# Performance work log

Hardware: AMD Instinct MI355X
Metric: run time of the kernel (lower is better)

The kernel has to match this reference:

```python
import jax, jax.numpy as jnp
import numpy as np

B_T = 32      # input capsule types
C_T = 32      # output capsule types
K = 3         # conv kernel
STRIDE = 2
H = 4         # pose matrix side
HH = H * H
ITERS = 3
EPS = 1e-10
LN_2PI = np.float32(np.log(2.0 * np.pi))


def setup_inputs() -> dict:
    key = jax.random.key(0)
    k1, k2, k3, k4, k5 = jax.random.split(key, 5)
    b, win = 16, 14
    poses = jax.random.normal(k1, (b, HH * B_T, win, win), dtype=jnp.float32)
    activations = jax.random.uniform(k2, (b, B_T, win, win), dtype=jnp.float32)
    W = jax.random.normal(k3, (B_T, K, K, C_T, H, H), dtype=jnp.float32)
    beta_v = jax.random.normal(k4, (1, C_T, 1, 1), dtype=jnp.float32)
    beta_a = jax.random.normal(k5, (1, C_T, 1), dtype=jnp.float32)
    lambda_ = jnp.float32(0.01)
    return {"lambda_": lambda_, "poses": poses, "activations": activations,
            "W": W, "beta_v": beta_v, "beta_a": beta_a}


def _em_routing(lambda_, a_in, V, beta_v, beta_a, b, Bkk, Cww, ww):
    sg = jax.lax.stop_gradient
    R = jnp.full((b, Bkk, Cww), 1.0 / C_T, dtype=V.dtype)
    a = mu = None
    for i in range(ITERS):
        R4 = (R * a_in)[..., None]                       # (b,Bkk,Cww,1)
        sum_R = R4.sum(1)                                # (b,Cww,1)
        mu = ((R4 * V).sum(1) / sum_R)[:, None]          # (b,1,Cww,hh)
        sigma_sq = ((R4 * (V - mu) ** 2).sum(1) / sum_R)[:, None]
        cost = (beta_v + jnp.log(jnp.sqrt(sigma_sq).reshape(b, C_T, ww, HH) + EPS)) \
               * sum_R.reshape(b, C_T, ww, 1)            # (b,C,ww,hh)
        a = jax.nn.sigmoid(lambda_ * (beta_a - cost.sum(-1)))  # (b,C,ww)
        a = a.reshape(b, Cww)
        if i != ITERS - 1:
            Vd, mud, ssd = sg(V), sg(mu), sg(sigma_sq)
            ln_p = -(Vd - mud) ** 2 / (2.0 * ssd) - jnp.log(jnp.sqrt(ssd)) - 0.5 * LN_2PI
            p = jnp.exp(ln_p)                            # (b,Bkk,Cww,hh)
            ap = sg(a)[:, None, :] * p.sum(-1)           # (b,Bkk,Cww)
            R = sg(ap / (ap.sum(2, keepdims=True) + EPS) + EPS)
    return a, mu


def _forward(lambda_, poses, activations, W, beta_v, beta_a):
    b, win = poses.shape[0], poses.shape[2]
    w = (win - K) // STRIDE + 1
    ww = w * w
    Bkk = K * K * B_T
    Cww = ww * C_T
    pose = poses.reshape(b, HH, B_T, win, win).transpose(0, 2, 3, 4, 1)
    # patch extraction indices: row ri[i, ki] = stride*i + ki
    ri = (STRIDE * np.arange(w))[:, None] + np.arange(K)  # (w, K)
    P = pose[:, :, ri]
    P = P[:, :, :, :, ri]         # (b,B,w_i,K_i,w_j,K_j,hh)
    # stack order in torch: dim=-1 index = j*w + i, patch dims (K_i,K_j,hh)
    patches = P.transpose(0, 1, 3, 5, 6, 4, 2).reshape(b, B_T, K, K, HH, ww)
    # faithful to torch .view (row-major reinterpretation mixing hh and ww)
    poses_r = patches.reshape(b, B_T, K, K, 1, w, w, H, H)
    W_hat = W[None, :, :, :, :, None, None, :, :]          # (1,B,K,K,C,1,1,h,h)
    votes = jnp.matmul(W_hat, poses_r)                     # (b,B,K,K,C,w,w,h,h)
    # activation patches, same (j*w+i) ordering
    A = activations[:, :, ri]
    A = A[:, :, :, :, ri]         # (b,B,w_i,K_i,w_j,K_j)
    act_p = A.transpose(0, 1, 3, 5, 4, 2).reshape(b, B_T, K, K, ww)
    a_ = jnp.broadcast_to(act_p.reshape(b, Bkk, 1, ww), (b, Bkk, C_T, ww)).reshape(b, Bkk, Cww)
    V = votes.reshape(b, Bkk, Cww, HH)
    a, mu = _em_routing(lambda_, a_, V, beta_v, beta_a, b, Bkk, Cww, ww)
    return mu.reshape(b, C_T, w, w, HH), a.reshape(b, C_T, w, w)


def reference(lambda_, poses, activations, W, beta_v, beta_a):
    return _forward(lambda_, poses, activations, W, beta_v, beta_a)
```

## Files before the change

kernel.cpp:

```cpp
#include <hip/hip_runtime.h>

#define EPS 1e-10f
#define HALF_LN2PI 0.91893853320467274f


template <int IT>
__global__ __launch_bounds__(256)
void m_pass(const float* __restrict__ poses, const float* __restrict__ acts,
            float* __restrict__ Ptg, float* __restrict__ actp,
            const float* __restrict__ W,
            const float* __restrict__ ap_buf, const float* __restrict__ denom_prev,
            float* __restrict__ Mpart)
{
    __shared__ __align__(16) float Pt_lds[1152];
    __shared__ float act_lds[72];
    __shared__ float invd_lds[72];
    __shared__ __align__(16) float red[128 * 18];

    const int tid  = threadIdx.x;
    const int wave = tid >> 6, lane = tid & 63;
    const int cl   = lane >> 2;
    const int bid  = blockIdx.x;
    const int blk  = bid >> 2, iq = bid & 3;
    const int bb   = blk / 36, p = blk - bb * 36;
    const int i0   = iq * 72;
    const size_t pbase  = (size_t)blk * 4608;
    const size_t apbase = (size_t)blk * 9216;

    if (IT == 0) {
        const int base = (p / 6) * 96 + (p % 6) * 16;
        for (int e = tid; e < 1152; e += 256) {
            int il = e >> 4, j = e & 15;
            int i = i0 + il;
            int hc = j >> 2, m = j & 3;
            int f = base + m * 4 + hc;
            int h = f / 36, sp = f - h * 36;
            int y = sp / 6, x = sp - y * 6;
            int B = i / 9, kk = i - B * 9;
            int ki = kk / 3, kj = kk - ki * 3;
            float v = poses[(size_t)((bb * 512 + h * 32 + B) * 14 + 2 * x + ki) * 14 + 2 * y + kj];
            Pt_lds[e] = v;
            Ptg[pbase + (size_t)i0 * 16 + e] = v;
        }
        const int y = p / 6, x = p - y * 6;
        for (int e = tid; e < 72; e += 256) {
            int i = i0 + e;
            int B = i / 9, kk = i - B * 9;
            int ki = kk / 3, kj = kk - ki * 3;
            float v = acts[(size_t)((bb * 32 + B) * 14 + 2 * x + ki) * 14 + 2 * y + kj];
            act_lds[e] = v;
            actp[blk * 288 + i] = v;
        }
    } else {
        const float4* src = (const float4*)(Ptg + pbase + (size_t)i0 * 16);
        float4* dst = (float4*)Pt_lds;
        for (int e = tid; e < 288; e += 256) dst[e] = src[e];
        for (int e = tid; e < 72; e += 256) {
            act_lds[e]  = actp[blk * 288 + i0 + e];
            invd_lds[e] = 1.0f / (denom_prev[bb * 288 + i0 + e] + EPS);
        }
    }
    __syncthreads();

    float acc[18];
#pragma unroll
    for (int k = 0; k < 18; ++k) acc[k] = 0.f;

    const float* Wt = W + (size_t)(i0 + wave * 18) * 512 + (lane << 2);
#pragma unroll 3
    for (int t = 0; t < 18; ++t) {
        const int il = wave * 18 + t;
        const float4 wva = *(const float4*)(Wt + (size_t)t * 512);
        const float4 wvb = *(const float4*)(Wt + (size_t)t * 512 + 256);
        float Ra, Rb;
        if (IT == 0) {
            Ra = 1.0f / 32.0f; Rb = 1.0f / 32.0f;
        } else {
            const int i = i0 + il;
            const float inv = invd_lds[il];
            Ra = fmaf(ap_buf[apbase + (size_t)i * 32 + cl],      inv, EPS);
            Rb = fmaf(ap_buf[apbase + (size_t)i * 32 + cl + 16], inv, EPS);
        }
        const float a_in = act_lds[il];
        const float R4a = Ra * a_in, R4b = Rb * a_in;
        acc[16] += R4a; acc[17] += R4b;
#pragma unroll
        for (int hc = 0; hc < 4; ++hc) {
            const float4 pv = *(const float4*)&Pt_lds[il * 16 + hc * 4];
            float Va = wva.x * pv.x + wva.y * pv.y + wva.z * pv.z + wva.w * pv.w;
            float Vb = wvb.x * pv.x + wvb.y * pv.y + wvb.z * pv.z + wvb.w * pv.w;
            acc[hc]      = fmaf(R4a, Va, acc[hc]);
            acc[4 + hc]  = fmaf(R4a * Va, Va, acc[4 + hc]);
            acc[8 + hc]  = fmaf(R4b, Vb, acc[8 + hc]);
            acc[12 + hc] = fmaf(R4b * Vb, Vb, acc[12 + hc]);
        }
    }

    if (wave >= 2) {
        float* d = &red[((wave - 2) * 64 + lane) * 18];
#pragma unroll
        for (int k = 0; k < 18; ++k) d[k] = acc[k];
    }
    __syncthreads();
    if (wave < 2) {
        const float* s = &red[(wave * 64 + lane) * 18];
#pragma unroll
        for (int k = 0; k < 18; ++k) acc[k] += s[k];
    }
    __syncthreads();
    if (wave == 1) {
        float* d = &red[lane * 18];
#pragma unroll
        for (int k = 0; k < 18; ++k) d[k] = acc[k];
    }
    __syncthreads();
    if (wave == 0) {
        const float* s = &red[lane * 18];
        float* mp = Mpart + (size_t)bid * 1152;
#pragma unroll
        for (int k = 0; k < 18; ++k) mp[k * 64 + lane] = acc[k] + s[k];
    }
}

__global__ __launch_bounds__(256)
void e_pass(const float* __restrict__ Ptg, const float* __restrict__ Mpart,
            const float* __restrict__ W, const float* __restrict__ beta_v,
            const float* __restrict__ beta_a, const float* __restrict__ lambda_p,
            float* __restrict__ ap_buf, float* __restrict__ denom_next)
{
    __shared__ __align__(16) float Pt_lds[1152];
    __shared__ float mu_s[512], n2_s[512], hl_s[512];
    __shared__ float a_s[32];

    const int tid  = threadIdx.x;
    const int wave = tid >> 6, lane = tid & 63;
    const int cl   = lane >> 2, hr = lane & 3;
    const int bid  = blockIdx.x;
    const int blk  = bid >> 2, iq = bid & 3;
    const int bb   = blk / 36;
    const int i0   = iq * 72;
    const size_t pbase  = (size_t)blk * 4608;
    const size_t apbase = (size_t)blk * 9216;

    {
        const float4* src = (const float4*)(Ptg + pbase + (size_t)i0 * 16);
        float4* dst = (float4*)Pt_lds;
        for (int e = tid; e < 288; e += 256) dst[e] = src[e];
    }

    if (wave == 0) {
        float s[18];
        const float* mp = Mpart + (size_t)blk * 4608;
#pragma unroll
        for (int k = 0; k < 18; ++k)
            s[k] = mp[k * 64 + lane] + mp[1152 + k * 64 + lane]
                 + mp[2304 + k * 64 + lane] + mp[3456 + k * 64 + lane];
        const float lam = lambda_p[0];
#pragma unroll
        for (int q = 0; q < 2; ++q) {
            const int c = cl + q * 16;
            const float sR = s[16 + q];
            float ls = 0.f;
#pragma unroll
            for (int hc = 0; hc < 4; ++hc) {
                const float S1 = s[q * 8 + hc];
                const float S2 = s[q * 8 + 4 + hc];
                const float mu = S1 / sR;
                float ss = S2 / sR - mu * mu;
                ss = fmaxf(ss, 1e-30f);
                const int ix = lane * 4 + q * 256 + hc;
                mu_s[ix] = mu;
                n2_s[ix] = -0.5f / ss;
                hl_s[ix] = -0.5f * __logf(ss) - HALF_LN2PI;
                ls += __logf(sqrtf(ss) + EPS);
            }
            ls += __shfl_xor(ls, 1);
            ls += __shfl_xor(ls, 2);
            const float cost = sR * (16.0f * beta_v[c] + ls);
            const float av = 1.0f / (1.0f + __expf(-lam * (beta_a[c] - cost)));
            if (hr == 0) a_s[c] = av;
        }
    }
    __syncthreads();

    const float aca = a_s[cl], acb = a_s[cl + 16];
    __align__(16) float mua[4], mub[4], na[4], nb[4], ha[4], hb[4];
    *(float4*)mua = *(const float4*)&mu_s[lane * 4];
    *(float4*)mub = *(const float4*)&mu_s[lane * 4 + 256];
    *(float4*)na  = *(const float4*)&n2_s[lane * 4];
    *(float4*)nb  = *(const float4*)&n2_s[lane * 4 + 256];
    *(float4*)ha  = *(const float4*)&hl_s[lane * 4];
    *(float4*)hb  = *(const float4*)&hl_s[lane * 4 + 256];

    const float* Wt = W + (size_t)(i0 + wave * 18) * 512 + (lane << 2);
#pragma unroll 3
    for (int t = 0; t < 18; ++t) {
        const int il = wave * 18 + t;
        const int i = i0 + il;
        const float4 wva = *(const float4*)(Wt + (size_t)t * 512);
        const float4 wvb = *(const float4*)(Wt + (size_t)t * 512 + 256);
        float pea = 0.f, peb = 0.f;
#pragma unroll
        for (int hc = 0; hc < 4; ++hc) {
            const float4 pv = *(const float4*)&Pt_lds[il * 16 + hc * 4];
            float Va = wva.x * pv.x + wva.y * pv.y + wva.z * pv.z + wva.w * pv.w;
            float Vb = wvb.x * pv.x + wvb.y * pv.y + wvb.z * pv.z + wvb.w * pv.w;
            float da = Va - mua[hc];
            float db = Vb - mub[hc];
            pea += __expf(fmaf(da * da, na[hc], ha[hc]));
            peb += __expf(fmaf(db * db, nb[hc], hb[hc]));
        }
        pea += __shfl_xor(pea, 1);
        pea += __shfl_xor(pea, 2);
        peb += __shfl_xor(peb, 1);
        peb += __shfl_xor(peb, 2);
        const float apa = aca * pea;
        const float apb = acb * peb;
        if (hr == 0) {
            ap_buf[apbase + (size_t)i * 32 + cl]      = apa;
            ap_buf[apbase + (size_t)i * 32 + cl + 16] = apb;
        }
        float dsum = apa + apb;
        dsum += __shfl_xor(dsum, 4);
        dsum += __shfl_xor(dsum, 8);
        dsum += __shfl_xor(dsum, 16);
        dsum += __shfl_xor(dsum, 32);
        if (lane == 0)
            atomicAdd(&denom_next[bb * 288 + i], dsum);
    }
}

__global__ __launch_bounds__(64)
void s_out(const float* __restrict__ Mpart, const float* __restrict__ beta_v,
           const float* __restrict__ beta_a, const float* __restrict__ lambda_p,
           float* __restrict__ d_out)
{
    const int lane = threadIdx.x;
    const int cl = lane >> 2, hr = lane & 3;
    const int blk = blockIdx.x;
    const int bb = blk / 36, p = blk - bb * 36;

    float s[18];
    const float* mp = Mpart + (size_t)blk * 4608;
#pragma unroll
    for (int k = 0; k < 18; ++k)
        s[k] = mp[k * 64 + lane] + mp[1152 + k * 64 + lane]
             + mp[2304 + k * 64 + lane] + mp[3456 + k * 64 + lane];

    const float lam = lambda_p[0];
#pragma unroll
    for (int q = 0; q < 2; ++q) {
        const int c = cl + q * 16;
        const float sR = s[16 + q];
        float ls = 0.f;
#pragma unroll
        for (int hc = 0; hc < 4; ++hc) {
            const float S1 = s[q * 8 + hc];
            const float S2 = s[q * 8 + 4 + hc];
            const float mu = S1 / sR;
            float ss = S2 / sR - mu * mu;
            ss = fmaxf(ss, 1e-30f);
            d_out[(size_t)bb * 18432 + (size_t)(c * 36 + p) * 16 + hr * 4 + hc] = mu;
            ls += __logf(sqrtf(ss) + EPS);
        }
        ls += __shfl_xor(ls, 1);
        ls += __shfl_xor(ls, 2);
        const float cost = sR * (16.0f * beta_v[c] + ls);
        const float av = 1.0f / (1.0f + __expf(-lam * (beta_a[c] - cost)));
        if (hr == 0)
            d_out[294912 + (size_t)bb * 1152 + c * 36 + p] = av;
    }
}

extern "C" void kernel_launch(void* const* d_in, const int* in_sizes, int n_in,
                              void* d_out, int out_size, void* d_ws, size_t ws_size,
                              hipStream_t stream)
{
    const float* lambda_p = (const float*)d_in[0];
    const float* poses    = (const float*)d_in[1];
    const float* acts     = (const float*)d_in[2];
    const float* W        = (const float*)d_in[3];
    const float* beta_v   = (const float*)d_in[4];
    const float* beta_a   = (const float*)d_in[5];
    float* out = (float*)d_out;

    float* ws     = (float*)d_ws;
    float* Ptg    = ws;
    float* actp   = Ptg + 2654208;
    float* ap_buf = actp + 165888;
    float* Mpart  = ap_buf + 5308416;
    float* denom0 = Mpart + 2654208;
    float* denom1 = denom0 + 4608;

    hipMemsetAsync(denom0, 0, 2 * 4608 * sizeof(float), stream);
    m_pass<0><<<2304, 256, 0, stream>>>(poses, acts, Ptg, actp, W, ap_buf, denom1, Mpart);
    e_pass<<<2304, 256, 0, stream>>>(Ptg, Mpart, W, beta_v, beta_a, lambda_p, ap_buf, denom0);
    m_pass<1><<<2304, 256, 0, stream>>>(poses, acts, Ptg, actp, W, ap_buf, denom0, Mpart);
    e_pass<<<2304, 256, 0, stream>>>(Ptg, Mpart, W, beta_v, beta_a, lambda_p, ap_buf, denom1);
    m_pass<2><<<2304, 256, 0, stream>>>(poses, acts, Ptg, actp, W, ap_buf, denom1, Mpart);
    s_out<<<576, 64, 0, stream>>>(Mpart, beta_v, beta_a, lambda_p, out);
}
```

Measured before the change: 190.7 us.

## Halve block size and hoist per-column statistics into separate finalize kernel

Blocks in m_pass and e_pass shrink from 256 to 128 threads, and each wave processes 36 input capsules instead of 18. This halves the cross-wave LDS reduction. The Mpart reduction and the mu/sigma/activation computation, previously redone by all four e_pass blocks per position, move into a small f_pass kernel that writes the statistics back into Mpart for e_pass to read. This removes redundant work but adds two extra kernel launches and fewer waves per block for latency hiding.

```diff
diff --git a/kernel.cpp b/kernel.cpp
--- a/kernel.cpp
+++ b/kernel.cpp
@@ -5,7 +5,7 @@
 
 
 template <int IT>
-__global__ __launch_bounds__(256)
+__global__ __launch_bounds__(128)
 void m_pass(const float* __restrict__ poses, const float* __restrict__ acts,
             float* __restrict__ Ptg, float* __restrict__ actp,
             const float* __restrict__ W,
@@ -15,7 +15,7 @@
     __shared__ __align__(16) float Pt_lds[1152];
     __shared__ float act_lds[72];
     __shared__ float invd_lds[72];
-    __shared__ __align__(16) float red[128 * 18];
+    __shared__ __align__(16) float red[1152];
 
     const int tid  = threadIdx.x;
     const int wave = tid >> 6, lane = tid & 63;
@@ -29,7 +29,7 @@
 
     if (IT == 0) {
         const int base = (p / 6) * 96 + (p % 6) * 16;
-        for (int e = tid; e < 1152; e += 256) {
+        for (int e = tid; e < 1152; e += 128) {
             int il = e >> 4, j = e & 15;
             int i = i0 + il;
             int hc = j >> 2, m = j & 3;
@@ -43,7 +43,7 @@
             Ptg[pbase + (size_t)i0 * 16 + e] = v;
         }
         const int y = p / 6, x = p - y * 6;
-        for (int e = tid; e < 72; e += 256) {
+        for (int e = tid; e < 72; e += 128) {
             int i = i0 + e;
             int B = i / 9, kk = i - B * 9;
             int ki = kk / 3, kj = kk - ki * 3;
@@ -54,8 +54,8 @@
     } else {
         const float4* src = (const float4*)(Ptg + pbase + (size_t)i0 * 16);
         float4* dst = (float4*)Pt_lds;
-        for (int e = tid; e < 288; e += 256) dst[e] = src[e];
-        for (int e = tid; e < 72; e += 256) {
+        for (int e = tid; e < 288; e += 128) dst[e] = src[e];
+        for (int e = tid; e < 72; e += 128) {
             act_lds[e]  = actp[blk * 288 + i0 + e];
             invd_lds[e] = 1.0f / (denom_prev[bb * 288 + i0 + e] + EPS);
         }
@@ -66,10 +66,10 @@
 #pragma unroll
     for (int k = 0; k < 18; ++k) acc[k] = 0.f;
 
-    const float* Wt = W + (size_t)(i0 + wave * 18) * 512 + (lane << 2);
-#pragma unroll 3
-    for (int t = 0; t < 18; ++t) {
-        const int il = wave * 18 + t;
+    const float* Wt = W + (size_t)(i0 + wave * 36) * 512 + (lane << 2);
+#pragma unroll 6
+    for (int t = 0; t < 36; ++t) {
+        const int il = wave * 36 + t;
         const float4 wva = *(const float4*)(Wt + (size_t)t * 512);
         const float4 wvb = *(const float4*)(Wt + (size_t)t * 512 + 256);
         float Ra, Rb;
@@ -96,41 +96,94 @@
         }
     }
 
-    if (wave >= 2) {
-        float* d = &red[((wave - 2) * 64 + lane) * 18];
-#pragma unroll
-        for (int k = 0; k < 18; ++k) d[k] = acc[k];
-    }
-    __syncthreads();
-    if (wave < 2) {
-        const float* s = &red[(wave * 64 + lane) * 18];
-#pragma unroll
-        for (int k = 0; k < 18; ++k) acc[k] += s[k];
-    }
-    __syncthreads();
     if (wave == 1) {
-        float* d = &red[lane * 18];
-#pragma unroll
-        for (int k = 0; k < 18; ++k) d[k] = acc[k];
+#pragma unroll
+        for (int k = 0; k < 18; ++k) red[lane * 18 + k] = acc[k];
     }
     __syncthreads();
     if (wave == 0) {
-        const float* s = &red[lane * 18];
         float* mp = Mpart + (size_t)bid * 1152;
 #pragma unroll
-        for (int k = 0; k < 18; ++k) mp[k * 64 + lane] = acc[k] + s[k];
-    }
-}
-
-__global__ __launch_bounds__(256)
+        for (int k = 0; k < 18; ++k)
+            mp[k * 64 + lane] = acc[k] + red[lane * 18 + k];
+    }
+}
+
+template <int FINAL>
+__global__ __launch_bounds__(64)
+void f_pass(float* __restrict__ Mpart, const float* __restrict__ beta_v,
+            const float* __restrict__ beta_a, const float* __restrict__ lambda_p,
+            float* __restrict__ d_out)
+{
+    const int lane = threadIdx.x;
+    const int cl = lane >> 2, hr = lane & 3;
+    const int blk = blockIdx.x;
+    const int bb = blk / 36, p = blk - bb * 36;
+    float* mp = Mpart + (size_t)blk * 4608;
+
+    float s[18];
+#pragma unroll
+    for (int k = 0; k < 18; ++k)
+        s[k] = mp[k * 64 + lane] + mp[1152 + k * 64 + lane]
+             + mp[2304 + k * 64 + lane] + mp[3456 + k * 64 + lane];
+
+    const float lam = lambda_p[0];
+    float muv[8], n2v[8], hlv[8], av[2];
+#pragma unroll
+    for (int q = 0; q < 2; ++q) {
+        const int c = cl + q * 16;
+        const float sR = s[16 + q];
+        float ls = 0.f;
+#pragma unroll
+        for (int hc = 0; hc < 4; ++hc) {
+            const float S1 = s[q * 8 + hc];
+            const float S2 = s[q * 8 + 4 + hc];
+            const float mu = S1 / sR;
+            float ss = S2 / sR - mu * mu;
+            ss = fmaxf(ss, 1e-30f);
+            muv[q * 4 + hc] = mu;
+            n2v[q * 4 + hc] = -0.5f / ss;
+            hlv[q * 4 + hc] = -0.5f * __logf(ss) - HALF_LN2PI;
+            ls += __logf(sqrtf(ss) + EPS);
+        }
+        ls += __shfl_xor(ls, 1);
+        ls += __shfl_xor(ls, 2);
+        const float cost = sR * (16.0f * beta_v[c] + ls);
+        av[q] = 1.0f / (1.0f + __expf(-lam * (beta_a[c] - cost)));
+    }
+
+    if (FINAL) {
+#pragma unroll
+        for (int q = 0; q < 2; ++q) {
+            const int c = cl + q * 16;
+#pragma unroll
+            for (int hc = 0; hc < 4; ++hc)
+                d_out[(size_t)bb * 18432 + (size_t)(c * 36 + p) * 16 + hr * 4 + hc] = muv[q * 4 + hc];
+            if (hr == 0)
+                d_out[294912 + (size_t)bb * 1152 + c * 36 + p] = av[q];
+        }
+    } else {
+        asm volatile("s_waitcnt vmcnt(0)" ::: "memory");
+#pragma unroll
+        for (int q = 0; q < 2; ++q) {
+#pragma unroll
+            for (int hc = 0; hc < 4; ++hc) {
+                const int ix = lane * 4 + q * 256 + hc;
+                mp[ix]        = muv[q * 4 + hc];
+                mp[512 + ix]  = n2v[q * 4 + hc];
+                mp[1024 + ix] = hlv[q * 4 + hc];
+            }
+            if (hr == 0) mp[1536 + cl + q * 16] = av[q];
+        }
+    }
+}
+
+__global__ __launch_bounds__(128)
 void e_pass(const float* __restrict__ Ptg, const float* __restrict__ Mpart,
-            const float* __restrict__ W, const float* __restrict__ beta_v,
-            const float* __restrict__ beta_a, const float* __restrict__ lambda_p,
+            const float* __restrict__ W,
             float* __restrict__ ap_buf, float* __restrict__ denom_next)
 {
     __shared__ __align__(16) float Pt_lds[1152];
-    __shared__ float mu_s[512], n2_s[512], hl_s[512];
-    __shared__ float a_s[32];
 
     const int tid  = threadIdx.x;
     const int wave = tid >> 6, lane = tid & 63;
@@ -145,57 +198,24 @@
     {
         const float4* src = (const float4*)(Ptg + pbase + (size_t)i0 * 16);
         float4* dst = (float4*)Pt_lds;
-        for (int e = tid; e < 288; e += 256) dst[e] = src[e];
-    }
-
-    if (wave == 0) {
-        float s[18];
-        const float* mp = Mpart + (size_t)blk * 4608;
-#pragma unroll
-        for (int k = 0; k < 18; ++k)
-            s[k] = mp[k * 64 + lane] + mp[1152 + k * 64 + lane]
-                 + mp[2304 + k * 64 + lane] + mp[3456 + k * 64 + lane];
-        const float lam = lambda_p[0];
-#pragma unroll
-        for (int q = 0; q < 2; ++q) {
-            const int c = cl + q * 16;
-            const float sR = s[16 + q];
-            float ls = 0.f;
-#pragma unroll
-            for (int hc = 0; hc < 4; ++hc) {
-                const float S1 = s[q * 8 + hc];
-                const float S2 = s[q * 8 + 4 + hc];
-                const float mu = S1 / sR;
-                float ss = S2 / sR - mu * mu;
-                ss = fmaxf(ss, 1e-30f);
-                const int ix = lane * 4 + q * 256 + hc;
-                mu_s[ix] = mu;
-                n2_s[ix] = -0.5f / ss;
-                hl_s[ix] = -0.5f * __logf(ss) - HALF_LN2PI;
-                ls += __logf(sqrtf(ss) + EPS);
-            }
-            ls += __shfl_xor(ls, 1);
-            ls += __shfl_xor(ls, 2);
-            const float cost = sR * (16.0f * beta_v[c] + ls);
-            const float av = 1.0f / (1.0f + __expf(-lam * (beta_a[c] - cost)));
-            if (hr == 0) a_s[c] = av;
-        }
-    }
+        for (int e = tid; e < 288; e += 128) dst[e] = src[e];
+    }
+
+    const float* st = Mpart + (size_t)blk * 4608;
+    __align__(16) float mua[4], mub[4], na[4], nb[4], ha[4], hb[4];
+    *(float4*)mua = *(const float4*)&st[lane * 4];
+    *(float4*)mub = *(const float4*)&st[lane * 4 + 256];
+    *(float4*)na  = *(const float4*)&st[512 + lane * 4];
+    *(float4*)nb  = *(const float4*)&st[512 + lane * 4 + 256];
+    *(float4*)ha  = *(const float4*)&st[1024 + lane * 4];
+    *(float4*)hb  = *(const float4*)&st[1024 + lane * 4 + 256];
+    const float aca = st[1536 + cl], acb = st[1536 + cl + 16];
     __syncthreads();
 
-    const float aca = a_s[cl], acb = a_s[cl + 16];
-    __align__(16) float mua[4], mub[4], na[4], nb[4], ha[4], hb[4];
-    *(float4*)mua = *(const float4*)&mu_s[lane * 4];
-    *(float4*)mub = *(const float4*)&mu_s[lane * 4 + 256];
-    *(float4*)na  = *(const float4*)&n2_s[lane * 4];
-    *(float4*)nb  = *(const float4*)&n2_s[lane * 4 + 256];
-    *(float4*)ha  = *(const float4*)&hl_s[lane * 4];
-    *(float4*)hb  = *(const float4*)&hl_s[lane * 4 + 256];
-
-    const float* Wt = W + (size_t)(i0 + wave * 18) * 512 + (lane << 2);
-#pragma unroll 3
-    for (int t = 0; t < 18; ++t) {
-        const int il = wave * 18 + t;
+    const float* Wt = W + (size_t)(i0 + wave * 36) * 512 + (lane << 2);
+#pragma unroll 6
+    for (int t = 0; t < 36; ++t) {
+        const int il = wave * 36 + t;
         const int i = i0 + il;
         const float4 wva = *(const float4*)(Wt + (size_t)t * 512);
         const float4 wvb = *(const float4*)(Wt + (size_t)t * 512 + 256);
@@ -230,48 +250,6 @@
     }
 }
 
-__global__ __launch_bounds__(64)
-void s_out(const float* __restrict__ Mpart, const float* __restrict__ beta_v,
-           const float* __restrict__ beta_a, const float* __restrict__ lambda_p,
-           float* __restrict__ d_out)
-{
-    const int lane = threadIdx.x;
-    const int cl = lane >> 2, hr = lane & 3;
-    const int blk = blockIdx.x;
-    const int bb = blk / 36, p = blk - bb * 36;
-
-    float s[18];
-    const float* mp = Mpart + (size_t)blk * 4608;
-#pragma unroll
-    for (int k = 0; k < 18; ++k)
-        s[k] = mp[k * 64 + lane] + mp[1152 + k * 64 + lane]
-             + mp[2304 + k * 64 + lane] + mp[3456 + k * 64 + lane];
-
-    const float lam = lambda_p[0];
-#pragma unroll
-    for (int q = 0; q < 2; ++q) {
-        const int c = cl + q * 16;
-        const float sR = s[16 + q];
-        float ls = 0.f;
-#pragma unroll
-        for (int hc = 0; hc < 4; ++hc) {
-            const float S1 = s[q * 8 + hc];
-            const float S2 = s[q * 8 + 4 + hc];
-            const float mu = S1 / sR;
-            float ss = S2 / sR - mu * mu;
-            ss = fmaxf(ss, 1e-30f);
-            d_out[(size_t)bb * 18432 + (size_t)(c * 36 + p) * 16 + hr * 4 + hc] = mu;
-            ls += __logf(sqrtf(ss) + EPS);
-        }
-        ls += __shfl_xor(ls, 1);
-        ls += __shfl_xor(ls, 2);
-        const float cost = sR * (16.0f * beta_v[c] + ls);
-        const float av = 1.0f / (1.0f + __expf(-lam * (beta_a[c] - cost)));
-        if (hr == 0)
-            d_out[294912 + (size_t)bb * 1152 + c * 36 + p] = av;
-    }
-}
-
 extern "C" void kernel_launch(void* const* d_in, const int* in_sizes, int n_in,
                               void* d_out, int out_size, void* d_ws, size_t ws_size,
                               hipStream_t stream)
@@ -293,10 +271,12 @@
     float* denom1 = denom0 + 4608;
 
     hipMemsetAsync(denom0, 0, 2 * 4608 * sizeof(float), stream);
-    m_pass<0><<<2304, 256, 0, stream>>>(poses, acts, Ptg, actp, W, ap_buf, denom1, Mpart);
-    e_pass<<<2304, 256, 0, stream>>>(Ptg, Mpart, W, beta_v, beta_a, lambda_p, ap_buf, denom0);
-    m_pass<1><<<2304, 256, 0, stream>>>(poses, acts, Ptg, actp, W, ap_buf, denom0, Mpart);
-    e_pass<<<2304, 256, 0, stream>>>(Ptg, Mpart, W, beta_v, beta_a, lambda_p, ap_buf, denom1);
-    m_pass<2><<<2304, 256, 0, stream>>>(poses, acts, Ptg, actp, W, ap_buf, denom1, Mpart);
-    s_out<<<576, 64, 0, stream>>>(Mpart, beta_v, beta_a, lambda_p, out);
-}
+    m_pass<0><<<2304, 128, 0, stream>>>(poses, acts, Ptg, actp, W, ap_buf, denom1, Mpart);
+    f_pass<0><<<576, 64, 0, stream>>>(Mpart, beta_v, beta_a, lambda_p, out);
+    e_pass<<<2304, 128, 0, stream>>>(Ptg, Mpart, W, ap_buf, denom0);
+    m_pass<1><<<2304, 128, 0, stream>>>(poses, acts, Ptg, actp, W, ap_buf, denom0, Mpart);
+    f_pass<0><<<576, 64, 0, stream>>>(Mpart, beta_v, beta_a, lambda_p, out);
+    e_pass<<<2304, 128, 0, stream>>>(Ptg, Mpart, W, ap_buf, denom1);
+    m_pass<2><<<2304, 128, 0, stream>>>(poses, acts, Ptg, actp, W, ap_buf, denom1, Mpart);
+    f_pass<1><<<576, 64, 0, stream>>>(Mpart, beta_v, beta_a, lambda_p, out);
+}
```

Measured after the change: 199.6 us. 1.05x slower.
